# Kernel optimization log

Measured on AMD Instinct MI355X. Metric: run time of the kernel, lower is better.

The kernel has to match this reference:

```python
import jax, jax.numpy as jnp
import numpy as np

BLOCKS = 16
TEMP = 0.7
SINK_ITERS = 8
CUT = 8
GUMBEL_EPS = 1e-6
IN_EPS = 1e-5
NEG = -1e9  # stands in for log(0) = -inf; exp(NEG) == 0 in fp32, avoids nan grads


def setup_inputs() -> dict:
    key = jax.random.key(0)
    k1, k2, k3 = jax.random.split(key, 3)
    shape = (8, 512, 4096, 1)  # [B, C, H, W=1]
    return {
        "q": jax.random.normal(k1, shape, jnp.float32),
        "k": jax.random.normal(k2, shape, jnp.float32),
        "v": jax.random.normal(k3, shape, jnp.float32),
    }


def _block_cat(x, blocks):
    # torch: cat(x.chunk(blocks, dim=2)[:-1], dim=-1)
    # [B,C,H,W] -> [B,C,H/blocks,(blocks-1)*W]
    B, C, H, W = x.shape
    Hb = H // blocks
    xb = x.reshape(B, C, blocks, Hb, W)[:, :, : blocks - 1]  # drop last chunk
    return jnp.transpose(xb, (0, 1, 3, 2, 4)).reshape(B, C, Hb, (blocks - 1) * W)


def reference(q, k, v):
    B, C, H, W = q.shape
    Hb = H // BLOCKS
    N = BLOCKS - 1  # number of retained blocks

    b_q = _block_cat(q, BLOCKS)  # [B,C,Hb,N]
    b_k = _block_cat(k, BLOCKS)
    b_v = _block_cat(v, BLOCKS)

    # ---- AttentionPermMatrix: Gumbel-Sinkhorn soft permutation [B,N,N] ----
    sq = jnp.swapaxes(b_q.mean(axis=1), 1, 2)  # [B,N,Hb]
    sk = jnp.swapaxes(b_k.mean(axis=1), 1, 2)
    R = jnp.einsum('bie,bje->bij', sq, sk) * (C ** -0.5)  # [B,N,N]
    Rp = jax.nn.relu(R)
    pos = R > 0
    r = jnp.where(pos, jnp.log(jnp.where(pos, Rp, 1.0)), NEG)  # safe log(relu(R))
    u = jax.random.uniform(jax.random.key(42), r.shape, r.dtype)
    gumbel = -jnp.log(-jnp.log(u + GUMBEL_EPS) + GUMBEL_EPS)
    r = (r + gumbel) / TEMP
    for _ in range(SINK_ITERS):
        r = r - jax.nn.logsumexp(r, axis=2, keepdims=True)
        r = r - jax.nn.logsumexp(r, axis=1, keepdims=True)
    perm = jnp.exp(r)  # [B,N,N]

    # ---- permute blocks of k/v (perm broadcast over channel dim C) ----
    k_sort = jnp.einsum('bchn,bnm->bchm', b_k, perm)  # [B,C,Hb,N]
    v_sort = jnp.einsum('bchn,bnm->bchm', b_v, perm)

    # ---- cut: first CUT size-1 chunks along last dim, cat along dim=-2, transpose(1,3)
    def cut(x):
        # [B,C,Hb,N] -> [B,C,CUT*Hb,1] (chunk j occupies rows j*Hb:(j+1)*Hb) -> [B,1,CUT*Hb,C]
        xc = jnp.transpose(x[..., :CUT], (0, 1, 3, 2)).reshape(B, C, CUT * Hb, 1)
        return jnp.transpose(xc, (0, 3, 2, 1))

    k_cut = cut(k_sort)  # [B,1,M,C], M = CUT*Hb
    v_cut = cut(v_sort)
    q_t = jnp.transpose(q, (0, 3, 2, 1))  # [B,1,H,C]

    logits = jnp.einsum('bwhc,bwmc->bwhm', q_t, k_cut) / TEMP  # [B,1,H,M]
    attn = jax.nn.softmax(logits, axis=-1)
    val = jnp.einsum('bwhm,bwmc->bwhc', attn, v_cut)  # [B,1,H,C]

    # InstanceNorm2d (affine=False): normalize over spatial dims (2,3) per (B, channel)
    mu = val.mean(axis=(2, 3), keepdims=True)
    var = val.var(axis=(2, 3), keepdims=True)
    return (val - mu) / jnp.sqrt(var + IN_EPS)
```

## Files before the change

kernel.cpp:

```cpp
#include <hip/hip_runtime.h>
#include <stdint.h>

typedef _Float16 half_t;
typedef _Float16 half8 __attribute__((ext_vector_type(8)));
typedef float floatx4 __attribute__((ext_vector_type(4)));

#define B_ 8
#define C_ 512
#define H_ 4096
#define HB 256
#define NB 15
#define CUT_ 8
#define M_ 2048
#define INV_TEMP (1.0f/0.7f)
#define NEG (-1e9f)

#define KROW 528
#define KT_BYTES 33792u
#define VT_BYTES 32768u

#define SQ_OFFB   0u
#define SK_OFFB   122880u
#define ST_OFFB   245760u
#define PERM_OFFB 245824u
#define KC16_OFFB 262144u
#define VC16_OFFB (262144u + 17301504u)
#define WS_NEED   (262144u + 17301504u + 16777216u)

__device__ __forceinline__ unsigned rotl32(unsigned x, unsigned n) {
    return (x << n) | (x >> (32u - n));
}
__device__ __forceinline__ void threefry2x32(unsigned k0, unsigned k1,
                                             unsigned x0, unsigned x1,
                                             unsigned &o0, unsigned &o1) {
    unsigned k2 = 0x1BD11BDAu ^ k0 ^ k1;
    x0 += k0; x1 += k1;
    x0+=x1; x1=rotl32(x1,13); x1^=x0;
    x0+=x1; x1=rotl32(x1,15); x1^=x0;
    x0+=x1; x1=rotl32(x1,26); x1^=x0;
    x0+=x1; x1=rotl32(x1, 6); x1^=x0;
    x0+=k1; x1+=k2+1u;
    x0+=x1; x1=rotl32(x1,17); x1^=x0;
    x0+=x1; x1=rotl32(x1,29); x1^=x0;
    x0+=x1; x1=rotl32(x1,16); x1^=x0;
    x0+=x1; x1=rotl32(x1,24); x1^=x0;
    x0+=k2; x1+=k0+2u;
    x0+=x1; x1=rotl32(x1,13); x1^=x0;
    x0+=x1; x1=rotl32(x1,15); x1^=x0;
    x0+=x1; x1=rotl32(x1,26); x1^=x0;
    x0+=x1; x1=rotl32(x1, 6); x1^=x0;
    x0+=k0; x1+=k1+3u;
    x0+=x1; x1=rotl32(x1,17); x1^=x0;
    x0+=x1; x1=rotl32(x1,29); x1^=x0;
    x0+=x1; x1=rotl32(x1,16); x1^=x0;
    x0+=x1; x1=rotl32(x1,24); x1^=x0;
    x0+=k1; x1+=k2+4u;
    x0+=x1; x1=rotl32(x1,13); x1^=x0;
    x0+=x1; x1=rotl32(x1,15); x1^=x0;
    x0+=x1; x1=rotl32(x1,26); x1^=x0;
    x0+=x1; x1=rotl32(x1, 6); x1^=x0;
    x0+=k2; x1+=k0+5u;
    o0 = x0; o1 = x1;
}

__device__ __forceinline__ void stage_tile(const char* gsrc, char* lbase,
                                           int w, int lane, int nchunk) {
    #pragma unroll
    for (int i = 0; i < 9; i++) {
        int cc = w + 4*i;
        if (cc < nchunk) {
            __builtin_amdgcn_global_load_lds(
                (const __attribute__((address_space(1))) void*)(uintptr_t)
                    (gsrc + (size_t)cc*1024u + (size_t)lane*16u),
                (__attribute__((address_space(3))) void*)(uintptr_t)
                    (lbase + (size_t)cc*1024u),
                16, 0, 0);
        }
    }
}

__global__ void colmean_kernel(const float* __restrict__ q, const float* __restrict__ k,
                               float* __restrict__ sq, float* __restrict__ sk) {
    int id  = blockIdx.x * 256 + threadIdx.x;
    int h   = id % 3840;
    int rest= id / 3840;
    int b   = rest % 8;
    int seg = rest / 8;
    int c0  = seg * 64;
    const float* qb = q + ((size_t)b*C_ + c0) * H_ + h;
    const float* kb = k + ((size_t)b*C_ + c0) * H_ + h;
    float aq = 0.f, ak = 0.f;
    #pragma unroll 8
    for (int c = 0; c < 64; c++) {
        aq += qb[(size_t)c * H_];
        ak += kb[(size_t)c * H_];
    }
    atomicAdd(&sq[b*3840 + h], aq * (1.0f/512.0f));
    atomicAdd(&sk[b*3840 + h], ak * (1.0f/512.0f));
}

__global__ void perm_kernel(const float* __restrict__ sqg, const float* __restrict__ skg,
                            float* __restrict__ perm) {
    int b = blockIdx.x;
    int tid = threadIdx.x;
    __shared__ float sqs[NB*HB];
    __shared__ float sks[NB*HB];
    __shared__ float mat[NB][16];
    __shared__ float lse[NB];
    for (int i = tid; i < NB*HB; i += 256) {
        sqs[i] = sqg[b*3840 + i];
        sks[i] = skg[b*3840 + i];
    }
    __syncthreads();
    int i = tid / 15, j = tid % 15;
    if (tid < 225) {
        float acc = 0.f;
        for (int h = 0; h < HB; h++) acc += sqs[i*HB + h] * sks[j*HB + h];
        float R = acc * 0.044194173824159216f;
        float r0 = (R > 0.0f) ? logf(R) : NEG;
        int g = (b*15 + i)*15 + j;
        unsigned o0, o1;
        threefry2x32(0u, 42u, 0u, (unsigned)g, o0, o1);
        unsigned bits = o0 ^ o1;
        float u = __uint_as_float((bits >> 9) | 0x3f800000u) - 1.0f;
        float gum = -logf(-logf(u + 1e-6f) + 1e-6f);
        mat[i][j] = (r0 + gum) * INV_TEMP;
    }
    __syncthreads();
    for (int it = 0; it < 8; it++) {
        if (tid < 15) {
            float m = -3.4e38f;
            for (int jj = 0; jj < 15; jj++) m = fmaxf(m, mat[tid][jj]);
            float s = 0.f;
            for (int jj = 0; jj < 15; jj++) s += expf(mat[tid][jj] - m);
            lse[tid] = m + logf(s);
        }
        __syncthreads();
        if (tid < 225) mat[i][j] -= lse[i];
        __syncthreads();
        if (tid < 15) {
            float m = -3.4e38f;
            for (int ii = 0; ii < 15; ii++) m = fmaxf(m, mat[ii][tid]);
            float s = 0.f;
            for (int ii = 0; ii < 15; ii++) s += expf(mat[ii][tid] - m);
            lse[tid] = m + logf(s);
        }
        __syncthreads();
        if (tid < 225) mat[i][j] -= lse[j];
        __syncthreads();
    }
    if (tid < 225) perm[b*225 + tid] = expf(mat[i][j]);
}

__global__ __launch_bounds__(256)
void kcut_kernel(const float* __restrict__ k, const float* __restrict__ perm,
                 half_t* __restrict__ kc) {
    int bid = blockIdx.x;
    int b = bid >> 4;
    int hch = (bid >> 1) & 7;
    int chalf = bid & 1;
    int h0 = hch * 32;
    int tid = threadIdx.x;
    __shared__ float kt[32*481];
    __shared__ float pl[NB][CUT_];
    if (tid < NB*CUT_) pl[tid/CUT_][tid%CUT_] = perm[b*225 + (tid/CUT_)*15 + (tid%CUT_)];
    int cp = tid & 31;
    int hg = tid >> 5;
    for (int ct = 0; ct < 8; ct++) {
        int c0 = chalf*256 + ct*32;
        __syncthreads();
        for (int it = 0; it < 15; it++) {
            int slot = tid + it*256;
            int h4 = slot & 7;
            int n  = (slot >> 3) % 15;
            int cc = slot / 120;
            float4 vv = *(const float4*)&k[((size_t)(b*C_ + c0 + cc))*H_ + n*HB + h0 + h4*4];
            *(float4*)&kt[cc*481 + n*32 + h4*4] = vv;
        }
        __syncthreads();
        float acc[CUT_][4];
        #pragma unroll
        for (int j = 0; j < CUT_; j++) { acc[j][0]=0.f; acc[j][1]=0.f; acc[j][2]=0.f; acc[j][3]=0.f; }
        #pragma unroll
        for (int n = 0; n < NB; n++) {
            float kv0 = kt[cp*481 + n*32 + hg*4 + 0];
            float kv1 = kt[cp*481 + n*32 + hg*4 + 1];
            float kv2 = kt[cp*481 + n*32 + hg*4 + 2];
            float kv3 = kt[cp*481 + n*32 + hg*4 + 3];
            #pragma unroll
            for (int j = 0; j < CUT_; j++) {
                float p = pl[n][j];
                acc[j][0] += kv0*p; acc[j][1] += kv1*p; acc[j][2] += kv2*p; acc[j][3] += kv3*p;
            }
        }
        #pragma unroll
        for (int j = 0; j < CUT_; j++)
            for (int q2 = 0; q2 < 4; q2++) {
                int m = j*HB + h0 + hg*4 + q2;
                kc[(((size_t)b*64 + (m>>5))*32 + (m&31))*KROW + c0 + cp] = (half_t)acc[j][q2];
            }
    }
}

__global__ __launch_bounds__(256)
void vcut_kernel(const float* __restrict__ v, const float* __restrict__ perm,
                 half_t* __restrict__ vc) {
    int bc = blockIdx.x;
    int b = bc >> 9;
    int c = bc & 511;
    int h = threadIdx.x;
    __shared__ float pl[NB][CUT_];
    if (h < NB*CUT_) pl[h/CUT_][h%CUT_] = perm[b*225 + (h/CUT_)*15 + (h%CUT_)];
    __syncthreads();
    const float* vb = v + (size_t)bc * H_ + h;
    float av[CUT_] = {0,0,0,0,0,0,0,0};
    #pragma unroll
    for (int n = 0; n < NB; n++) {
        float vv = vb[n*HB];
        #pragma unroll
        for (int j = 0; j < CUT_; j++) av[j] += vv * pl[n][j];
    }
    #pragma unroll
    for (int j = 0; j < CUT_; j++)
        vc[(((size_t)b*64 + j*8 + (h>>5))*512 + c)*32 + (h&31)] = (half_t)av[j];
}

__global__ __launch_bounds__(256, 2)
void attn_kernel(const float* __restrict__ q, const half_t* __restrict__ kc,
                 const half_t* __restrict__ vc, float* __restrict__ out,
                 float* __restrict__ stats) {
    __shared__ half_t ktile[32][KROW];
    __shared__ half_t vtile[512][32];
    __shared__ float  spart[2][32][34];
    __shared__ half_t pslab[2][32][40];
    __shared__ float  redbuf[4][2];

    int bid = blockIdx.x;
    int b   = bid & 7;
    int h0  = (bid >> 3) * 32;
    int tid = threadIdx.x;
    int w    = tid >> 6;
    int lane = tid & 63;
    int lm   = lane & 15;
    int quad = lane >> 4;
    int wm = w & 1;
    int wc = w >> 1;

    float (*qstage)[68] = reinterpret_cast<float(*)[68]>(&spart[0][0][0]);

    half8 qhi[8], qlo[8];
    for (int ch = 0; ch < 8; ch++) {
        int c0 = ch * 64;
        __syncthreads();
        #pragma unroll
        for (int it = 0; it < 2; it++) {
            int slot = tid + it*256;
            int cc = slot >> 3;
            int h4 = slot & 7;
            float4 qv = *(const float4*)&q[((size_t)(b*C_ + c0 + cc))*H_ + h0 + h4*4];
            qstage[h4*4+0][cc] = qv.x;
            qstage[h4*4+1][cc] = qv.y;
            qstage[h4*4+2][cc] = qv.z;
            qstage[h4*4+3][cc] = qv.w;
        }
        __syncthreads();
        if ((ch >> 2) == wc) {
            int row = 16*wm + lm;
            #pragma unroll
            for (int kk = 0; kk < 2; kk++) {
                int kb = (ch & 3)*2 + kk;
                const float* qp = &qstage[row][kk*32 + quad*8];
                float4 a = *(const float4*)qp;
                float4 c4 = *(const float4*)(qp + 4);
                float vals[8] = {a.x,a.y,a.z,a.w,c4.x,c4.y,c4.z,c4.w};
                half8 hh, hl;
                #pragma unroll
                for (int j = 0; j < 8; j++) {
                    float xv = vals[j] * INV_TEMP;
                    half_t h1 = (half_t)xv;
                    hh[j] = h1;
                    hl[j] = (half_t)(xv - (float)h1);
                }
                qhi[kb] = hh; qlo[kb] = hl;
            }
        }
    }

    floatx4 O[16];
    #pragma unroll
    for (int n = 0; n < 16; n++) O[n] = (floatx4)0.f;
    floatx4 Ol = (floatx4)0.f;
    float ms[4] = {-3.4e38f,-3.4e38f,-3.4e38f,-3.4e38f};
    half8 vone;
    #pragma unroll
    for (int j = 0; j < 8; j++) vone[j] = (half_t)1.0f;

    const char* kbytes = (const char*)kc + (size_t)b * 64u * KT_BYTES;
    const char* vbytes = (const char*)vc + (size_t)b * 64u * VT_BYTES;

    stage_tile(kbytes, (char*)&ktile[0][0], w, lane, 33);

    int rbase = 16*wm + quad*4;

    for (int t = 0; t < 64; t++) {
        __syncthreads();
        stage_tile(vbytes + (size_t)t*VT_BYTES, (char*)&vtile[0][0], w, lane, 32);

        floatx4 acc0 = (floatx4)0.f, acc1 = (floatx4)0.f;
        #pragma unroll
        for (int kb = 0; kb < 8; kb++) {
            int coff = 256*wc + 32*kb + quad*8;
            half8 b0 = *(const half8*)&ktile[lm][coff];
            half8 b1 = *(const half8*)&ktile[16 + lm][coff];
            acc0 = __builtin_amdgcn_mfma_f32_16x16x32_f16(qhi[kb], b0, acc0, 0, 0, 0);
            acc0 = __builtin_amdgcn_mfma_f32_16x16x32_f16(qlo[kb], b0, acc0, 0, 0, 0);
            acc1 = __builtin_amdgcn_mfma_f32_16x16x32_f16(qhi[kb], b1, acc1, 0, 0, 0);
            acc1 = __builtin_amdgcn_mfma_f32_16x16x32_f16(qlo[kb], b1, acc1, 0, 0, 0);
        }
        #pragma unroll
        for (int r = 0; r < 4; r++) {
            spart[wc][rbase + r][lm]      = acc0[r];
            spart[wc][rbase + r][16 + lm] = acc1[r];
        }
        __syncthreads();
        if (t + 1 < 64)
            stage_tile(kbytes + (size_t)(t+1)*KT_BYTES, (char*)&ktile[0][0], w, lane, 33);

        float s0[4], s1[4], mxv[4];
        int need = 0;
        #pragma unroll
        for (int r = 0; r < 4; r++) {
            s0[r] = spart[0][rbase+r][lm]    + spart[1][rbase+r][lm];
            s1[r] = spart[0][rbase+r][16+lm] + spart[1][rbase+r][16+lm];
            float m2 = fmaxf(s0[r], s1[r]);
            #pragma unroll
            for (int msk = 1; msk < 16; msk <<= 1) m2 = fmaxf(m2, __shfl_xor(m2, msk, 16));
            mxv[r] = m2;
            need |= (m2 > ms[r] + 8.0f) ? 1 : 0;
        }
        if (__any(need)) {
            #pragma unroll
            for (int r = 0; r < 4; r++) {
                float mn = fmaxf(ms[r], mxv[r]);
                float al = __expf(ms[r] - mn);
                ms[r] = mn;
                Ol[r] *= al;
                #pragma unroll
                for (int n = 0; n < 16; n++) O[n][r] *= al;
            }
        }
        #pragma unroll
        for (int r = 0; r < 4; r++) {
            pslab[wc][rbase + r][lm]      = (half_t)__expf(s0[r] - ms[r]);
            pslab[wc][rbase + r][16 + lm] = (half_t)__expf(s1[r] - ms[r]);
        }
        half8 pa = *(const half8*)&pslab[wc][16*wm + lm][quad*8];
        #pragma unroll
        for (int n = 0; n < 16; n++) {
            half8 vb = *(const half8*)&vtile[256*wc + 16*n + lm][quad*8];
            O[n] = __builtin_amdgcn_mfma_f32_16x16x32_f16(pa, vb, O[n], 0, 0, 0);
        }
        Ol = __builtin_amdgcn_mfma_f32_16x16x32_f16(pa, vone, Ol, 0, 0, 0);
    }

    float inv4[4];
    #pragma unroll
    for (int r = 0; r < 4; r++) inv4[r] = 1.0f / Ol[r];
    float sa = 0.f, sb = 0.f;
    int rowg = h0 + rbase;
    #pragma unroll
    for (int n = 0; n < 16; n++) {
        #pragma unroll
        for (int r = 0; r < 4; r++) {
            float o = O[n][r] * inv4[r];
            out[((size_t)b*H_ + rowg + r)*C_ + 256*wc + 16*n + lm] = o;
            sa += o; sb += o*o;
        }
    }
    #pragma unroll
    for (int msk = 1; msk < 64; msk <<= 1) {
        sa += __shfl_xor(sa, msk, 64);
        sb += __shfl_xor(sb, msk, 64);
    }
    if (lane == 0) { redbuf[w][0] = sa; redbuf[w][1] = sb; }
    __syncthreads();
    if (tid == 0) {
        float a = 0.f, c2 = 0.f;
        for (int w2 = 0; w2 < 4; w2++) { a += redbuf[w2][0]; c2 += redbuf[w2][1]; }
        atomicAdd(&stats[b*2    ], a);
        atomicAdd(&stats[b*2 + 1], c2);
    }
}

__global__ void norm_kernel(float* __restrict__ out, const float* __restrict__ stats) {
    size_t i = (size_t)blockIdx.x * 256 + threadIdx.x;
    int b = (int)(i >> 19);
    float4 vv = ((float4*)out)[i];
    const float inv = 1.0f / (4096.0f * 512.0f);
    float mu  = stats[b*2] * inv;
    float var = stats[b*2 + 1] * inv - mu*mu;
    float rs  = rsqrtf(var + 1e-5f);
    vv.x = (vv.x - mu) * rs;
    vv.y = (vv.y - mu) * rs;
    vv.z = (vv.z - mu) * rs;
    vv.w = (vv.w - mu) * rs;
    ((float4*)out)[i] = vv;
}

extern "C" void kernel_launch(void* const* d_in, const int* in_sizes, int n_in,
                              void* d_out, int out_size, void* d_ws, size_t ws_size,
                              hipStream_t stream) {
    const float* q = (const float*)d_in[0];
    const float* k = (const float*)d_in[1];
    const float* v = (const float*)d_in[2];
    float* out = (float*)d_out;
    if (ws_size < (size_t)WS_NEED) return;

    float*  sq    = (float*) ((char*)d_ws + SQ_OFFB);
    float*  sk    = (float*) ((char*)d_ws + SK_OFFB);
    float*  stats = (float*) ((char*)d_ws + ST_OFFB);
    float*  perm  = (float*) ((char*)d_ws + PERM_OFFB);
    half_t* kc    = (half_t*)((char*)d_ws + KC16_OFFB);
    half_t* vc    = (half_t*)((char*)d_ws + VC16_OFFB);

    hipMemsetAsync(d_ws, 0, (size_t)KC16_OFFB, stream);

    colmean_kernel<<<960,  256, 0, stream>>>(q, k, sq, sk);
    perm_kernel   <<<8,    256, 0, stream>>>(sq, sk, perm);
    kcut_kernel   <<<128,  256, 0, stream>>>(k, perm, kc);
    vcut_kernel   <<<4096, 256, 0, stream>>>(v, perm, vc);
    attn_kernel   <<<1024, 256, 0, stream>>>(q, kc, vc, out, stats);
    norm_kernel   <<<16384,256, 0, stream>>>(out, stats);
}
```

Before: 650.3 us.

## Double-buffer K tiles, load V to registers, transpose QK MFMA, widen kcut grid

The attention kernel now double-buffers the K tile in shared memory and prefetches the next tile before the QK MFMAs. V fragments are read straight from global memory into registers instead of being staged through LDS. The QK MFMA operands are swapped so each lane holds one query row, which makes the running max a single scalar per lane reduced with two cross-lane shuffles, and setprio hints are added around the MFMA blocks. The kcut kernel splits its channel loop across 8x more blocks to raise parallelism. The tradeoffs are more LDS per block, which may limit occupancy, and uncoalesced-ish direct V register loads.

```diff
diff --git a/kernel.cpp b/kernel.cpp
--- a/kernel.cpp
+++ b/kernel.cpp
@@ -155,10 +155,11 @@
 __global__ __launch_bounds__(256)
 void kcut_kernel(const float* __restrict__ k, const float* __restrict__ perm,
                  half_t* __restrict__ kc) {
-    int bid = blockIdx.x;
-    int b = bid >> 4;
-    int hch = (bid >> 1) & 7;
-    int chalf = bid & 1;
+    int bid  = blockIdx.x;
+    int ct   = bid & 7;
+    int chalf= (bid >> 3) & 1;
+    int hch  = (bid >> 4) & 7;
+    int b    = bid >> 7;
     int h0 = hch * 32;
     int tid = threadIdx.x;
     __shared__ float kt[32*481];
@@ -166,40 +167,37 @@
     if (tid < NB*CUT_) pl[tid/CUT_][tid%CUT_] = perm[b*225 + (tid/CUT_)*15 + (tid%CUT_)];
     int cp = tid & 31;
     int hg = tid >> 5;
-    for (int ct = 0; ct < 8; ct++) {
-        int c0 = chalf*256 + ct*32;
-        __syncthreads();
-        for (int it = 0; it < 15; it++) {
-            int slot = tid + it*256;
-            int h4 = slot & 7;
-            int n  = (slot >> 3) % 15;
-            int cc = slot / 120;
-            float4 vv = *(const float4*)&k[((size_t)(b*C_ + c0 + cc))*H_ + n*HB + h0 + h4*4];
-            *(float4*)&kt[cc*481 + n*32 + h4*4] = vv;
-        }
-        __syncthreads();
-        float acc[CUT_][4];
-        #pragma unroll
-        for (int j = 0; j < CUT_; j++) { acc[j][0]=0.f; acc[j][1]=0.f; acc[j][2]=0.f; acc[j][3]=0.f; }
-        #pragma unroll
-        for (int n = 0; n < NB; n++) {
-            float kv0 = kt[cp*481 + n*32 + hg*4 + 0];
-            float kv1 = kt[cp*481 + n*32 + hg*4 + 1];
-            float kv2 = kt[cp*481 + n*32 + hg*4 + 2];
-            float kv3 = kt[cp*481 + n*32 + hg*4 + 3];
-            #pragma unroll
-            for (int j = 0; j < CUT_; j++) {
-                float p = pl[n][j];
-                acc[j][0] += kv0*p; acc[j][1] += kv1*p; acc[j][2] += kv2*p; acc[j][3] += kv3*p;
-            }
-        }
-        #pragma unroll
-        for (int j = 0; j < CUT_; j++)
-            for (int q2 = 0; q2 < 4; q2++) {
-                int m = j*HB + h0 + hg*4 + q2;
-                kc[(((size_t)b*64 + (m>>5))*32 + (m&31))*KROW + c0 + cp] = (half_t)acc[j][q2];
-            }
-    }
+    int c0 = chalf*256 + ct*32;
+    for (int it = 0; it < 15; it++) {
+        int slot = tid + it*256;
+        int h4 = slot & 7;
+        int n  = (slot >> 3) % 15;
+        int cc = slot / 120;
+        float4 vv = *(const float4*)&k[((size_t)(b*C_ + c0 + cc))*H_ + n*HB + h0 + h4*4];
+        *(float4*)&kt[cc*481 + n*32 + h4*4] = vv;
+    }
+    __syncthreads();
+    float acc[CUT_][4];
+    #pragma unroll
+    for (int j = 0; j < CUT_; j++) { acc[j][0]=0.f; acc[j][1]=0.f; acc[j][2]=0.f; acc[j][3]=0.f; }
+    #pragma unroll
+    for (int n = 0; n < NB; n++) {
+        float kv0 = kt[cp*481 + n*32 + hg*4 + 0];
+        float kv1 = kt[cp*481 + n*32 + hg*4 + 1];
+        float kv2 = kt[cp*481 + n*32 + hg*4 + 2];
+        float kv3 = kt[cp*481 + n*32 + hg*4 + 3];
+        #pragma unroll
+        for (int j = 0; j < CUT_; j++) {
+            float p = pl[n][j];
+            acc[j][0] += kv0*p; acc[j][1] += kv1*p; acc[j][2] += kv2*p; acc[j][3] += kv3*p;
+        }
+    }
+    #pragma unroll
+    for (int j = 0; j < CUT_; j++)
+        for (int q2 = 0; q2 < 4; q2++) {
+            int m = j*HB + h0 + hg*4 + q2;
+            kc[(((size_t)b*64 + (m>>5))*32 + (m&31))*KROW + c0 + cp] = (half_t)acc[j][q2];
+        }
 }
 
 __global__ __launch_bounds__(256)
@@ -229,8 +227,7 @@
 void attn_kernel(const float* __restrict__ q, const half_t* __restrict__ kc,
                  const half_t* __restrict__ vc, float* __restrict__ out,
                  float* __restrict__ stats) {
-    __shared__ half_t ktile[32][KROW];
-    __shared__ half_t vtile[512][32];
+    __shared__ half_t ktile[2][32][KROW];
     __shared__ float  spart[2][32][34];
     __shared__ half_t pslab[2][32][40];
     __shared__ float  redbuf[4][2];
@@ -245,6 +242,13 @@
     int quad = lane >> 4;
     int wm = w & 1;
     int wc = w >> 1;
+    int row = 16*wm + lm;
+    int key0 = 4*quad;
+
+    const char* kbytes = (const char*)kc + (size_t)b * 64u * KT_BYTES;
+    const char* vbytes = (const char*)vc + (size_t)b * 64u * VT_BYTES;
+
+    stage_tile(kbytes, (char*)&ktile[0][0][0], w, lane, 33);
 
     float (*qstage)[68] = reinterpret_cast<float(*)[68]>(&spart[0][0][0]);
 
@@ -265,7 +269,6 @@
         }
         __syncthreads();
         if ((ch >> 2) == wc) {
-            int row = 16*wm + lm;
             #pragma unroll
             for (int kk = 0; kk < 2; kk++) {
                 int kb = (ch & 3)*2 + kk;
@@ -290,84 +293,90 @@
     #pragma unroll
     for (int n = 0; n < 16; n++) O[n] = (floatx4)0.f;
     floatx4 Ol = (floatx4)0.f;
-    float ms[4] = {-3.4e38f,-3.4e38f,-3.4e38f,-3.4e38f};
+    float ms = -3.4e38f;
     half8 vone;
     #pragma unroll
     for (int j = 0; j < 8; j++) vone[j] = (half_t)1.0f;
 
-    const char* kbytes = (const char*)kc + (size_t)b * 64u * KT_BYTES;
-    const char* vbytes = (const char*)vc + (size_t)b * 64u * VT_BYTES;
-
-    stage_tile(kbytes, (char*)&ktile[0][0], w, lane, 33);
-
-    int rbase = 16*wm + quad*4;
-
+    int buf = 0;
     for (int t = 0; t < 64; t++) {
         __syncthreads();
-        stage_tile(vbytes + (size_t)t*VT_BYTES, (char*)&vtile[0][0], w, lane, 32);
+        half8 vreg[16];
+        {
+            const half_t* vt = (const half_t*)(vbytes + (size_t)t*VT_BYTES);
+            #pragma unroll
+            for (int n = 0; n < 16; n++)
+                vreg[n] = *(const half8*)(vt + (256*wc + 16*n + lm)*32 + quad*8);
+        }
+        if (t + 1 < 64)
+            stage_tile(kbytes + (size_t)(t+1)*KT_BYTES, (char*)&ktile[buf^1][0][0], w, lane, 33);
 
         floatx4 acc0 = (floatx4)0.f, acc1 = (floatx4)0.f;
+        __builtin_amdgcn_s_setprio(1);
         #pragma unroll
         for (int kb = 0; kb < 8; kb++) {
             int coff = 256*wc + 32*kb + quad*8;
-            half8 b0 = *(const half8*)&ktile[lm][coff];
-            half8 b1 = *(const half8*)&ktile[16 + lm][coff];
-            acc0 = __builtin_amdgcn_mfma_f32_16x16x32_f16(qhi[kb], b0, acc0, 0, 0, 0);
-            acc0 = __builtin_amdgcn_mfma_f32_16x16x32_f16(qlo[kb], b0, acc0, 0, 0, 0);
-            acc1 = __builtin_amdgcn_mfma_f32_16x16x32_f16(qhi[kb], b1, acc1, 0, 0, 0);
-            acc1 = __builtin_amdgcn_mfma_f32_16x16x32_f16(qlo[kb], b1, acc1, 0, 0, 0);
-        }
+            half8 a0 = *(const half8*)&ktile[buf][lm][coff];
+            half8 a1 = *(const half8*)&ktile[buf][16 + lm][coff];
+            acc0 = __builtin_amdgcn_mfma_f32_16x16x32_f16(a0, qhi[kb], acc0, 0, 0, 0);
+            acc0 = __builtin_amdgcn_mfma_f32_16x16x32_f16(a0, qlo[kb], acc0, 0, 0, 0);
+            acc1 = __builtin_amdgcn_mfma_f32_16x16x32_f16(a1, qhi[kb], acc1, 0, 0, 0);
+            acc1 = __builtin_amdgcn_mfma_f32_16x16x32_f16(a1, qlo[kb], acc1, 0, 0, 0);
+        }
+        __builtin_amdgcn_s_setprio(0);
         #pragma unroll
         for (int r = 0; r < 4; r++) {
-            spart[wc][rbase + r][lm]      = acc0[r];
-            spart[wc][rbase + r][16 + lm] = acc1[r];
-        }
-        __syncthreads();
-        if (t + 1 < 64)
-            stage_tile(kbytes + (size_t)(t+1)*KT_BYTES, (char*)&ktile[0][0], w, lane, 33);
-
-        float s0[4], s1[4], mxv[4];
-        int need = 0;
+            spart[wc][key0 + r][row]      = acc0[r];
+            spart[wc][16 + key0 + r][row] = acc1[r];
+        }
+        asm volatile("s_waitcnt lgkmcnt(0)\n\ts_barrier" ::: "memory");
+
+        float s0[4], s1[4];
         #pragma unroll
         for (int r = 0; r < 4; r++) {
-            s0[r] = spart[0][rbase+r][lm]    + spart[1][rbase+r][lm];
-            s1[r] = spart[0][rbase+r][16+lm] + spart[1][rbase+r][16+lm];
-            float m2 = fmaxf(s0[r], s1[r]);
+            s0[r] = acc0[r] + spart[wc^1][key0 + r][row];
+            s1[r] = acc1[r] + spart[wc^1][16 + key0 + r][row];
+        }
+        float m2 = fmaxf(fmaxf(fmaxf(s0[0],s0[1]), fmaxf(s0[2],s0[3])),
+                         fmaxf(fmaxf(s1[0],s1[1]), fmaxf(s1[2],s1[3])));
+        m2 = fmaxf(m2, __shfl_xor(m2, 16, 64));
+        m2 = fmaxf(m2, __shfl_xor(m2, 32, 64));
+        int need = (m2 > ms + 8.0f) ? 1 : 0;
+        if (__any(need)) {
+            float mn = fmaxf(ms, m2);
+            float aown = __expf(ms - mn);
+            ms = mn;
+            float ar[4];
             #pragma unroll
-            for (int msk = 1; msk < 16; msk <<= 1) m2 = fmaxf(m2, __shfl_xor(m2, msk, 16));
-            mxv[r] = m2;
-            need |= (m2 > ms[r] + 8.0f) ? 1 : 0;
-        }
-        if (__any(need)) {
+            for (int r = 0; r < 4; r++) ar[r] = __shfl(aown, key0 + r, 64);
             #pragma unroll
-            for (int r = 0; r < 4; r++) {
-                float mn = fmaxf(ms[r], mxv[r]);
-                float al = __expf(ms[r] - mn);
-                ms[r] = mn;
-                Ol[r] *= al;
+            for (int r = 0; r < 4; r++) Ol[r] *= ar[r];
+            #pragma unroll
+            for (int n = 0; n < 16; n++) {
                 #pragma unroll
-                for (int n = 0; n < 16; n++) O[n][r] *= al;
+                for (int r = 0; r < 4; r++) O[n][r] *= ar[r];
             }
         }
         #pragma unroll
         for (int r = 0; r < 4; r++) {
-            pslab[wc][rbase + r][lm]      = (half_t)__expf(s0[r] - ms[r]);
-            pslab[wc][rbase + r][16 + lm] = (half_t)__expf(s1[r] - ms[r]);
-        }
-        half8 pa = *(const half8*)&pslab[wc][16*wm + lm][quad*8];
-        #pragma unroll
-        for (int n = 0; n < 16; n++) {
-            half8 vb = *(const half8*)&vtile[256*wc + 16*n + lm][quad*8];
-            O[n] = __builtin_amdgcn_mfma_f32_16x16x32_f16(pa, vb, O[n], 0, 0, 0);
-        }
+            pslab[wc][row][key0 + r]      = (half_t)__expf(s0[r] - ms);
+            pslab[wc][row][16 + key0 + r] = (half_t)__expf(s1[r] - ms);
+        }
+        half8 pa = *(const half8*)&pslab[wc][row][quad*8];
+        __builtin_amdgcn_s_setprio(1);
+        #pragma unroll
+        for (int n = 0; n < 16; n++)
+            O[n] = __builtin_amdgcn_mfma_f32_16x16x32_f16(pa, vreg[n], O[n], 0, 0, 0);
         Ol = __builtin_amdgcn_mfma_f32_16x16x32_f16(pa, vone, Ol, 0, 0, 0);
+        __builtin_amdgcn_s_setprio(0);
+        buf ^= 1;
     }
 
     float inv4[4];
     #pragma unroll
     for (int r = 0; r < 4; r++) inv4[r] = 1.0f / Ol[r];
     float sa = 0.f, sb = 0.f;
-    int rowg = h0 + rbase;
+    int rowg = h0 + 16*wm + quad*4;
     #pragma unroll
     for (int n = 0; n < 16; n++) {
         #pragma unroll
@@ -427,7 +436,7 @@
 
     colmean_kernel<<<960,  256, 0, stream>>>(q, k, sq, sk);
     perm_kernel   <<<8,    256, 0, stream>>>(sq, sk, perm);
-    kcut_kernel   <<<128,  256, 0, stream>>>(k, perm, kc);
+    kcut_kernel   <<<1024, 256, 0, stream>>>(k, perm, kc);
     vcut_kernel   <<<4096, 256, 0, stream>>>(v, perm, vc);
     attn_kernel   <<<1024, 256, 0, stream>>>(q, kc, vc, out, stats);
     norm_kernel   <<<16384,256, 0, stream>>>(out, stats);
```

Measured after the change: 628.1 us. 3.4% less time.
